# Optimization experiments

Measured on AMD Instinct MI355X. Metric: run time of the kernel, lower is better.

## Reference

```python
import jax, jax.numpy as jnp
import numpy as np

B, F, V, E, D_DENSE = 16384, 26, 100000, 16, 13
HIDDEN = [256, 128]
DNN_IN = F * E + D_DENSE  # 429
INIT_STD = 1e-4


def setup_inputs() -> dict:
    key = jax.random.key(0)
    ks = jax.random.split(key, 12)
    X_sparse = jax.random.randint(ks[0], (B, F), 0, V, dtype=jnp.int32)
    X_dense = jax.random.normal(ks[1], (B, D_DENSE), dtype=jnp.float32)
    # Per-field embedding tables stacked: [F, V, dim]
    lin_emb_w = jax.random.normal(ks[2], (F, V, 1), dtype=jnp.float32) * 0.01
    fm_emb_w = jax.random.normal(ks[3], (F, V, E), dtype=jnp.float32) * 0.01
    dense_w = jax.random.normal(ks[4], (1, D_DENSE), dtype=jnp.float32) * 0.01
    dense_b = jnp.zeros((1,), dtype=jnp.float32)
    W1 = jax.random.normal(ks[5], (HIDDEN[0], DNN_IN), dtype=jnp.float32) * INIT_STD
    b1 = jnp.zeros((HIDDEN[0],), dtype=jnp.float32)
    W2 = jax.random.normal(ks[6], (HIDDEN[1], HIDDEN[0]), dtype=jnp.float32) * INIT_STD
    b2 = jnp.zeros((HIDDEN[1],), dtype=jnp.float32)
    Wout = jax.random.normal(ks[7], (1, HIDDEN[1]), dtype=jnp.float32) * 0.01
    return {"X_sparse": X_sparse, "X_dense": X_dense, "lin_emb_w": lin_emb_w,
            "fm_emb_w": fm_emb_w, "dense_w": dense_w, "dense_b": dense_b,
            "W1": W1, "b1": b1, "W2": W2, "b2": b2, "Wout": Wout}


def reference(X_sparse, X_dense, lin_emb_w, fm_emb_w, dense_w, dense_b,
              W1, b1, W2, b2, Wout):
    f_idx = jnp.arange(F)[None, :]  # broadcast field index against [B, F]
    # --- FM linear (1st order) part ---
    lin_sparse = lin_emb_w[f_idx, X_sparse]            # [B, F, 1]
    lin_sparse = jnp.sum(lin_sparse, axis=1)           # [B, 1]
    lin_dense = X_dense @ dense_w.T + dense_b          # [B, 1]
    linear_part = lin_sparse + lin_dense
    # --- FM 2nd-order cross term ---
    fm = fm_emb_w[f_idx, X_sparse]                     # [B, F, E]
    sum_emb = jnp.sum(fm, axis=1)                      # [B, E]
    square_of_sum = sum_emb * sum_emb
    sum_of_square = jnp.sum(fm * fm, axis=1)
    cross = 0.5 * jnp.sum(square_of_sum - sum_of_square, axis=1, keepdims=True)
    fm_logit = linear_part + cross                     # [B, 1]
    # --- DNN part (dropout identity: eval mode) ---
    h = jnp.concatenate([fm.reshape(B, F * E), X_dense], axis=1)  # [B, 429]
    h = jax.nn.relu(h @ W1.T + b1)
    h = jax.nn.relu(h @ W2.T + b2)
    dnn_logit = h @ Wout.T                             # [B, 1]
    out = jax.nn.sigmoid(fm_logit + dnn_logit)
    return out.squeeze(1)                              # [B]
```

## Files before the change

kernel.cpp:

```cpp
#include <hip/hip_runtime.h>
#include <hip/hip_bf16.h>
#include <math.h>

#define BTOT   16384
#define NF     26
#define VOCAB  100000
#define EDIM   16
#define DD     13
#define KPAD   448
#define KREAL  429
#define N1     256
#define N2     128
#define SPB    64
#define APAD   456
#define H2PAD  264

typedef __attribute__((ext_vector_type(8))) short bf16x8;
typedef __attribute__((ext_vector_type(4))) short bf16x4;
typedef __attribute__((ext_vector_type(4))) float f32x4;

static __device__ __forceinline__ bf16x8 ldb8(const __hip_bfloat16* p) {
  return *reinterpret_cast<const bf16x8*>(p);
}
static __device__ __forceinline__ short f2bf(float f) {
  __hip_bfloat16 h = __float2bfloat16(f);
  return *reinterpret_cast<short*>(&h);
}

__global__ __launch_bounds__(512) void convert_weights(
    const float* __restrict__ W1, const float* __restrict__ W2,
    __hip_bfloat16* __restrict__ W1f, __hip_bfloat16* __restrict__ W2f) {
  const int bid = blockIdx.x;
  const int k = threadIdx.x;
  if (bid < 256) {
    const int n = bid;
    if (k < 448) {
      float v = (k < KREAL) ? W1[(size_t)n * KREAL + k] : 0.f;
      W1f[(((size_t)(k >> 3)) * N1 + n) * 8 + (k & 7)] = __float2bfloat16(v);
    }
  } else {
    const int n = bid - 256;
    if (k < 256) {
      float v = W2[(size_t)n * 256 + k];
      W2f[(((size_t)(k >> 3)) * N2 + n) * 8 + (k & 7)] = __float2bfloat16(v);
    }
  }
}

__global__ __launch_bounds__(1024, 4) void deepfm_fused(
    const int* __restrict__ Xs, const float* __restrict__ Xd,
    const float* __restrict__ linW, const float* __restrict__ fmW,
    const float* __restrict__ denseW, const float* __restrict__ denseB,
    const __hip_bfloat16* __restrict__ W1f, const float* __restrict__ b1,
    const __hip_bfloat16* __restrict__ W2f, const float* __restrict__ b2,
    const float* __restrict__ Wout, float* __restrict__ out) {

  __shared__ __hip_bfloat16 Ash[SPB][APAD];
  __shared__ __hip_bfloat16 H2sh[SPB][H2PAD];
  __shared__ float fmlsh[SPB];
  __shared__ float redsh[SPB][8];

  const int tid = threadIdx.x;
  const size_t blk0 = (size_t)blockIdx.x * SPB;

  {
    const int s   = tid >> 4;
    const int sub = tid & 15;
    const int q   = sub & 3;
    const int g   = sub >> 2;
    const size_t b = blk0 + s;
    const int* xrow = Xs + b * NF;

    int idxs[7];
#pragma unroll
    for (int i = 0; i < 7; ++i) {
      int f = g + 4 * i;
      idxs[i] = (f < NF) ? xrow[f] : 0;
    }

    f32x4 sum = (f32x4){0.f, 0.f, 0.f, 0.f};
    f32x4 sumsq = (f32x4){0.f, 0.f, 0.f, 0.f};
    float part = 0.f;

#pragma unroll
    for (int i = 0; i < 7; ++i) {
      const int f = g + 4 * i;
      if (f < NF) {
        const float* row = fmW + ((size_t)f * VOCAB + idxs[i]) * EDIM;
        f32x4 v = *reinterpret_cast<const f32x4*>(row + q * 4);
        sum += v;
        sumsq += v * v;
        bf16x4 pk;
        pk[0] = f2bf(v[0]); pk[1] = f2bf(v[1]);
        pk[2] = f2bf(v[2]); pk[3] = f2bf(v[3]);
        *reinterpret_cast<bf16x4*>(&Ash[s][f * EDIM + q * 4]) = pk;
        if (q == (i & 3))
          part += linW[(size_t)f * VOCAB + idxs[i]];
      }
    }
#pragma unroll
    for (int off = 4; off <= 8; off <<= 1) {
#pragma unroll
      for (int c = 0; c < 4; ++c) {
        sum[c] += __shfl_xor(sum[c], off);
        sumsq[c] += __shfl_xor(sumsq[c], off);
      }
    }
    if (g == 0) {
      f32x4 c4 = sum * sum - sumsq;
      part += 0.5f * (c4[0] + c4[1] + c4[2] + c4[3]);
    }
    float xd = (sub < DD) ? Xd[b * DD + sub] : 0.f;
    Ash[s][416 + sub] = __float2bfloat16(xd);
    Ash[s][432 + sub] = __float2bfloat16(0.f);
    if (sub < DD) part += xd * denseW[sub];
#pragma unroll
    for (int off = 1; off < 16; off <<= 1)
      part += __shfl_xor(part, off);
    if (sub == 0) fmlsh[s] = part + denseB[0];
  }
  __syncthreads();

  const int wave = tid >> 6;
  const int lane = tid & 63;
  const int lr = lane & 15;
  const int kg = lane >> 4;
  {
    const int n0 = wave * 16;
    f32x4 acc[4];
#pragma unroll
    for (int mt = 0; mt < 4; ++mt) acc[mt] = (f32x4){0.f, 0.f, 0.f, 0.f};

#pragma unroll
    for (int kt = 0; kt < KPAD / 32; ++kt) {
      const int kbase = kt * 32 + kg * 8;
      bf16x8 bf = ldb8(W1f + ((size_t)(kbase >> 3) * N1 + n0 + lr) * 8);
#pragma unroll
      for (int mt = 0; mt < 4; ++mt) {
        bf16x8 af = *reinterpret_cast<const bf16x8*>(&Ash[mt * 16 + lr][kbase]);
        acc[mt] = __builtin_amdgcn_mfma_f32_16x16x32_bf16(af, bf, acc[mt], 0, 0, 0);
      }
    }
    const int col = n0 + lr;
    const float bias = b1[col];
#pragma unroll
    for (int mt = 0; mt < 4; ++mt) {
#pragma unroll
      for (int r = 0; r < 4; ++r) {
        float v = acc[mt][r] + bias;
        v = v > 0.f ? v : 0.f;
        H2sh[mt * 16 + kg * 4 + r][col] = __float2bfloat16(v);
      }
    }
  }
  __syncthreads();

  {
    const int c  = wave & 7;
    const int h  = wave >> 3;
    const int n0 = c * 16;
    f32x4 acc[2];
    acc[0] = (f32x4){0.f, 0.f, 0.f, 0.f};
    acc[1] = (f32x4){0.f, 0.f, 0.f, 0.f};

#pragma unroll
    for (int kt = 0; kt < N1 / 32; ++kt) {
      const int kbase = kt * 32 + kg * 8;
      bf16x8 bf = ldb8(W2f + ((size_t)(kbase >> 3) * N2 + n0 + lr) * 8);
#pragma unroll
      for (int mt = 0; mt < 2; ++mt) {
        bf16x8 af = *reinterpret_cast<const bf16x8*>(&H2sh[h * 32 + mt * 16 + lr][kbase]);
        acc[mt] = __builtin_amdgcn_mfma_f32_16x16x32_bf16(af, bf, acc[mt], 0, 0, 0);
      }
    }
    const float w0 = Wout[n0 + lr];
    const float bb0 = b2[n0 + lr];
#pragma unroll
    for (int mt = 0; mt < 2; ++mt) {
#pragma unroll
      for (int r = 0; r < 4; ++r) {
        float v = acc[mt][r] + bb0;
        v = v > 0.f ? v : 0.f;
        v *= w0;
#pragma unroll
        for (int off = 1; off < 16; off <<= 1)
          v += __shfl_xor(v, off);
        if (lr == 0) redsh[h * 32 + mt * 16 + kg * 4 + r][c] = v;
      }
    }
  }
  __syncthreads();

  if (tid < SPB) {
    const int row = tid;
    float t = 0.f;
#pragma unroll
    for (int w = 0; w < 8; ++w) t += redsh[row][w];
    float x = fmlsh[row] + t;
    out[blk0 + row] = 1.f / (1.f + expf(-x));
  }
}

extern "C" void kernel_launch(void* const* d_in, const int* in_sizes, int n_in,
                              void* d_out, int out_size, void* d_ws, size_t ws_size,
                              hipStream_t stream) {
  const int*   Xs   = (const int*)d_in[0];
  const float* Xd   = (const float*)d_in[1];
  const float* linW = (const float*)d_in[2];
  const float* fmW  = (const float*)d_in[3];
  const float* dW   = (const float*)d_in[4];
  const float* dB   = (const float*)d_in[5];
  const float* W1   = (const float*)d_in[6];
  const float* b1   = (const float*)d_in[7];
  const float* W2   = (const float*)d_in[8];
  const float* b2   = (const float*)d_in[9];
  const float* Wout = (const float*)d_in[10];
  float* out = (float*)d_out;

  char* ws = (char*)d_ws;
  __hip_bfloat16* W1f = (__hip_bfloat16*)(ws);
  __hip_bfloat16* W2f = (__hip_bfloat16*)(ws + 229376);

  convert_weights<<<384, 512, 0, stream>>>(W1, W2, W1f, W2f);
  deepfm_fused<<<BTOT / SPB, 1024, 0, stream>>>(
      Xs, Xd, linW, fmW, dW, dB, W1f, b1, W2f, b2, Wout, out);
}
```

Baseline: 32.15 us.

## Split gather into separate kernel with smaller blocks, merging weight conversion

The embedding gather and FM computation move out of the fused GEMM kernel into a new kernel with 256-thread blocks, 16 samples each, so many more blocks are available to hide gather latency. The same kernel also performs the W1/W2 bf16 conversion, which removes one launch. The gathered bf16 activation matrix and FM logits go to a global workspace, and the GEMM kernel reloads them from there. The cost is an extra ~14 MB global write and read round trip for the activations.

```diff
diff --git a/kernel.cpp b/kernel.cpp
--- a/kernel.cpp
+++ b/kernel.cpp
@@ -27,97 +27,106 @@
   return *reinterpret_cast<short*>(&h);
 }
 
-__global__ __launch_bounds__(512) void convert_weights(
-    const float* __restrict__ W1, const float* __restrict__ W2,
-    __hip_bfloat16* __restrict__ W1f, __hip_bfloat16* __restrict__ W2f) {
-  const int bid = blockIdx.x;
-  const int k = threadIdx.x;
-  if (bid < 256) {
-    const int n = bid;
-    if (k < 448) {
-      float v = (k < KREAL) ? W1[(size_t)n * KREAL + k] : 0.f;
-      W1f[(((size_t)(k >> 3)) * N1 + n) * 8 + (k & 7)] = __float2bfloat16(v);
-    }
-  } else {
-    const int n = bid - 256;
-    if (k < 256) {
-      float v = W2[(size_t)n * 256 + k];
-      W2f[(((size_t)(k >> 3)) * N2 + n) * 8 + (k & 7)] = __float2bfloat16(v);
-    }
-  }
-}
-
-__global__ __launch_bounds__(1024, 4) void deepfm_fused(
+__global__ __launch_bounds__(256, 8) void gather_conv(
     const int* __restrict__ Xs, const float* __restrict__ Xd,
     const float* __restrict__ linW, const float* __restrict__ fmW,
     const float* __restrict__ denseW, const float* __restrict__ denseB,
+    const float* __restrict__ W1, const float* __restrict__ W2,
+    __hip_bfloat16* __restrict__ Aout, float* __restrict__ fml,
+    __hip_bfloat16* __restrict__ W1f, __hip_bfloat16* __restrict__ W2f) {
+  const int tid = threadIdx.x;
+  const int bid = blockIdx.x;
+
+  if (bid < 256) {
+    const int n = bid;
+    for (int kk = tid; kk < KPAD; kk += 256) {
+      float v = (kk < KREAL) ? W1[(size_t)n * KREAL + kk] : 0.f;
+      W1f[(((size_t)(kk >> 3)) * N1 + n) * 8 + (kk & 7)] = __float2bfloat16(v);
+    }
+  } else if (bid < 384) {
+    const int n = bid - 256;
+    float v = W2[(size_t)n * N1 + tid];
+    W2f[(((size_t)(tid >> 3)) * N2 + n) * 8 + (tid & 7)] = __float2bfloat16(v);
+  }
+
+  const int s   = tid >> 4;
+  const int sub = tid & 15;
+  const int q   = sub & 3;
+  const int g   = sub >> 2;
+  const size_t b = (size_t)bid * 16 + s;
+  const int* xrow = Xs + b * NF;
+
+  int idxs[7];
+#pragma unroll
+  for (int i = 0; i < 7; ++i) {
+    int f = g + 4 * i;
+    idxs[i] = (f < NF) ? xrow[f] : 0;
+  }
+
+  f32x4 sum = (f32x4){0.f, 0.f, 0.f, 0.f};
+  f32x4 sumsq = (f32x4){0.f, 0.f, 0.f, 0.f};
+  float part = 0.f;
+  __hip_bfloat16* arow = Aout + b * KPAD;
+
+#pragma unroll
+  for (int i = 0; i < 7; ++i) {
+    const int f = g + 4 * i;
+    if (f < NF) {
+      const float* row = fmW + ((size_t)f * VOCAB + idxs[i]) * EDIM;
+      f32x4 v = *reinterpret_cast<const f32x4*>(row + q * 4);
+      sum += v;
+      sumsq += v * v;
+      bf16x4 pk;
+      pk[0] = f2bf(v[0]); pk[1] = f2bf(v[1]);
+      pk[2] = f2bf(v[2]); pk[3] = f2bf(v[3]);
+      *reinterpret_cast<bf16x4*>(&arow[f * EDIM + q * 4]) = pk;
+      if (q == (i & 3))
+        part += linW[(size_t)f * VOCAB + idxs[i]];
+    }
+  }
+#pragma unroll
+  for (int off = 4; off <= 8; off <<= 1) {
+#pragma unroll
+    for (int c = 0; c < 4; ++c) {
+      sum[c] += __shfl_xor(sum[c], off);
+      sumsq[c] += __shfl_xor(sumsq[c], off);
+    }
+  }
+  if (g == 0) {
+    f32x4 c4 = sum * sum - sumsq;
+    part += 0.5f * (c4[0] + c4[1] + c4[2] + c4[3]);
+  }
+  float xd = (sub < DD) ? Xd[b * DD + sub] : 0.f;
+  arow[416 + sub] = __float2bfloat16(xd);
+  arow[432 + sub] = __float2bfloat16(0.f);
+  if (sub < DD) part += xd * denseW[sub];
+#pragma unroll
+  for (int off = 1; off < 16; off <<= 1)
+    part += __shfl_xor(part, off);
+  if (sub == 0) fml[b] = part + denseB[0];
+}
+
+__global__ __launch_bounds__(1024, 4) void gemm_fused(
+    const __hip_bfloat16* __restrict__ Aout, const float* __restrict__ fml,
     const __hip_bfloat16* __restrict__ W1f, const float* __restrict__ b1,
     const __hip_bfloat16* __restrict__ W2f, const float* __restrict__ b2,
     const float* __restrict__ Wout, float* __restrict__ out) {
 
   __shared__ __hip_bfloat16 Ash[SPB][APAD];
   __shared__ __hip_bfloat16 H2sh[SPB][H2PAD];
-  __shared__ float fmlsh[SPB];
   __shared__ float redsh[SPB][8];
 
   const int tid = threadIdx.x;
   const size_t blk0 = (size_t)blockIdx.x * SPB;
 
   {
-    const int s   = tid >> 4;
-    const int sub = tid & 15;
-    const int q   = sub & 3;
-    const int g   = sub >> 2;
-    const size_t b = blk0 + s;
-    const int* xrow = Xs + b * NF;
-
-    int idxs[7];
-#pragma unroll
-    for (int i = 0; i < 7; ++i) {
-      int f = g + 4 * i;
-      idxs[i] = (f < NF) ? xrow[f] : 0;
-    }
-
-    f32x4 sum = (f32x4){0.f, 0.f, 0.f, 0.f};
-    f32x4 sumsq = (f32x4){0.f, 0.f, 0.f, 0.f};
-    float part = 0.f;
-
-#pragma unroll
-    for (int i = 0; i < 7; ++i) {
-      const int f = g + 4 * i;
-      if (f < NF) {
-        const float* row = fmW + ((size_t)f * VOCAB + idxs[i]) * EDIM;
-        f32x4 v = *reinterpret_cast<const f32x4*>(row + q * 4);
-        sum += v;
-        sumsq += v * v;
-        bf16x4 pk;
-        pk[0] = f2bf(v[0]); pk[1] = f2bf(v[1]);
-        pk[2] = f2bf(v[2]); pk[3] = f2bf(v[3]);
-        *reinterpret_cast<bf16x4*>(&Ash[s][f * EDIM + q * 4]) = pk;
-        if (q == (i & 3))
-          part += linW[(size_t)f * VOCAB + idxs[i]];
-      }
-    }
-#pragma unroll
-    for (int off = 4; off <= 8; off <<= 1) {
-#pragma unroll
-      for (int c = 0; c < 4; ++c) {
-        sum[c] += __shfl_xor(sum[c], off);
-        sumsq[c] += __shfl_xor(sumsq[c], off);
-      }
-    }
-    if (g == 0) {
-      f32x4 c4 = sum * sum - sumsq;
-      part += 0.5f * (c4[0] + c4[1] + c4[2] + c4[3]);
-    }
-    float xd = (sub < DD) ? Xd[b * DD + sub] : 0.f;
-    Ash[s][416 + sub] = __float2bfloat16(xd);
-    Ash[s][432 + sub] = __float2bfloat16(0.f);
-    if (sub < DD) part += xd * denseW[sub];
-#pragma unroll
-    for (int off = 1; off < 16; off <<= 1)
-      part += __shfl_xor(part, off);
-    if (sub == 0) fmlsh[s] = part + denseB[0];
+#pragma unroll
+    for (int v = tid; v < SPB * 56; v += 1024) {
+      const int row = v / 56;
+      const int c8 = v - row * 56;
+      bf16x8 x = ldb8(Aout + (blk0 + row) * KPAD + c8 * 8);
+      *reinterpret_cast<bf16x8*>(&Ash[row][c8 * 8]) = x;
+    }
   }
   __syncthreads();
 
@@ -196,7 +205,7 @@
     float t = 0.f;
 #pragma unroll
     for (int w = 0; w < 8; ++w) t += redsh[row][w];
-    float x = fmlsh[row] + t;
+    float x = fml[blk0 + row] + t;
     out[blk0 + row] = 1.f / (1.f + expf(-x));
   }
 }
@@ -218,10 +227,13 @@
   float* out = (float*)d_out;
 
   char* ws = (char*)d_ws;
-  __hip_bfloat16* W1f = (__hip_bfloat16*)(ws);
-  __hip_bfloat16* W2f = (__hip_bfloat16*)(ws + 229376);
-
-  convert_weights<<<384, 512, 0, stream>>>(W1, W2, W1f, W2f);
-  deepfm_fused<<<BTOT / SPB, 1024, 0, stream>>>(
-      Xs, Xd, linW, fmW, dW, dB, W1f, b1, W2f, b2, Wout, out);
-}
+  __hip_bfloat16* A   = (__hip_bfloat16*)(ws);
+  float*          fml = (float*)(ws + 14680064);
+  __hip_bfloat16* W1f = (__hip_bfloat16*)(ws + 14745600);
+  __hip_bfloat16* W2f = (__hip_bfloat16*)(ws + 14974976);
+
+  gather_conv<<<BTOT / 16, 256, 0, stream>>>(
+      Xs, Xd, linW, fmW, dW, dB, W1, W2, A, fml, W1f, W2f);
+  gemm_fused<<<BTOT / SPB, 1024, 0, stream>>>(
+      A, fml, W1f, b1, W2f, b2, Wout, out);
+}
```

Result: slower. 33.91 us (+5.5%).
